# Optimization experiments

Hardware: AMD Instinct MI355X
Metric: run time of the kernel (lower is better)

## Reference

```python
import jax, jax.numpy as jnp
import numpy as np

WS = 3   # window_size
ND = 3   # n_degree


def grid_sample_bilinear(x, grid):
    """torch.nn.functional.grid_sample, mode='bilinear', padding_mode='zeros', align_corners=True.
    x: [B,C,H,W]; grid: [B,Hg,Wg,2] with grid[...,0]=x(norm), grid[...,1]=y(norm). -> [B,C,Hg,Wg]"""
    B, C, H, W = x.shape
    gx = (grid[..., 0] + 1.0) * 0.5 * (W - 1)
    gy = (grid[..., 1] + 1.0) * 0.5 * (H - 1)
    x0 = jnp.floor(gx); y0 = jnp.floor(gy)
    x1 = x0 + 1.0;      y1 = y0 + 1.0
    wx1 = gx - x0; wx0 = 1.0 - wx1
    wy1 = gy - y0; wy0 = 1.0 - wy1
    xf = x.reshape(B, C, H * W)

    def gather(yi, xi):
        valid = ((yi >= 0) & (yi <= H - 1) & (xi >= 0) & (xi <= W - 1)).astype(x.dtype)
        yc = jnp.clip(yi, 0, H - 1).astype(jnp.int32)
        xc = jnp.clip(xi, 0, W - 1).astype(jnp.int32)
        idx = yc * W + xc                                   # [B,Hg,Wg]
        v = jax.vmap(lambda xb, ib: jnp.take(xb, ib, axis=1))(xf, idx.reshape(B, -1))
        v = v.reshape(B, C, idx.shape[1], idx.shape[2])      # [B,C,Hg,Wg]
        return v * valid[:, None]

    out = (gather(y0, x0) * (wy0 * wx0)[:, None]
         + gather(y0, x1) * (wy0 * wx1)[:, None]
         + gather(y1, x0) * (wy1 * wx0)[:, None]
         + gather(y1, x1) * (wy1 * wx1)[:, None])
    return out


def setup_inputs() -> dict:
    key = jax.random.key(0)
    ks = jax.random.split(key, 8)
    B, Q, C, H, W = 16, 500, 256, 64, 64
    Np = ND + 1
    query = jax.random.normal(ks[0], (B, Q, C), dtype=jnp.float32)
    # polynomial coefficients kept small so most sample points land inside [-1,1]
    polys = jax.random.uniform(ks[1], (B, Q, 2 * Np), dtype=jnp.float32, minval=0.0, maxval=0.25)
    memory = jax.random.normal(ks[2], (B, H * W, C), dtype=jnp.float32)
    memory_spatial_shapes = np.array([[H, W]], dtype=np.int64)  # static shapes
    Wk = jax.random.normal(ks[3], (C, Np * C, WS, WS), dtype=jnp.float32) * 0.02
    bk = jax.random.normal(ks[4], (C,), dtype=jnp.float32) * 0.02
    Wp = jax.random.normal(ks[5], (C, C), dtype=jnp.float32) * 0.02
    bp = jax.random.normal(ks[6], (C,), dtype=jnp.float32) * 0.02
    return {"query": query, "polys": polys, "memory": memory,
            "memory_spatial_shapes": memory_spatial_shapes,
            "Wk": Wk, "bk": bk, "Wp": Wp, "bp": bp}


def reference(query, polys, memory, memory_spatial_shapes, Wk, bk, Wp, bp):
    B, LEN_V, C = memory.shape
    H = int(memory_spatial_shapes[0][0]); W = int(memory_spatial_shapes[0][1])
    Q = polys.shape[1]
    Np = ND + 1

    # memory -> feature map [B,C,H,W]
    x = jnp.transpose(memory[:, :H * W, :], (0, 2, 1)).reshape(B, C, H, W)

    # polynomial sample points: alphas[s,k] = linspace(0,1)[s] ** (ND-k)
    a = jnp.linspace(0.0, 1.0, Np).astype(polys.dtype)
    A = jnp.stack([a ** i for i in range(ND, -1, -1)], axis=1)          # [Np, Np]
    pts = jnp.einsum('bqck,sk->bqcs', polys.reshape(B, Q, 2, Np), A)    # [B,Q,2,Np]
    pts = jnp.transpose(pts, (0, 1, 3, 2))[..., ::-1]                   # [B,Q,Np,2] (flip coords)
    points = 2.0 * pts - 1.0
    points = points[:, :, None]                                         # [B,Q,1,Np,2]

    # window offsets (note python floor-div: (-3)//2 = -2, matches torch source)
    delta_h = 2.0 * jnp.linspace((-WS) // 2, WS // 2, WS) / H
    delta_w = 2.0 * jnp.linspace((-WS) // 2, WS // 2, WS) / W
    mesh_x, mesh_y = jnp.meshgrid(delta_w, delta_h, indexing='xy')       # [WS,WS]
    mesh_x = mesh_x.reshape(-1, 1); mesh_y = mesh_y.reshape(-1, 1)       # [WS*WS,1]

    grid_x = points[..., 1] + mesh_x                                     # [B,Q,WS*WS,Np]
    grid_y = points[..., 0] + mesh_y
    grid = jnp.stack((grid_y, grid_x), axis=-1)                          # [B,Q,WS*WS,Np,2]
    grid = grid.reshape(B, Q * Np * WS, WS, 2)

    sampled = grid_sample_bilinear(x, grid)                              # [B,C,Q*Np*WS,WS]
    sampled = sampled.reshape(B, C, Q * Np, WS, WS)
    sampled = jnp.transpose(sampled, (0, 2, 1, 3, 4)).reshape(B * Q, Np * C, WS, WS)

    # convkk over full window -> 1x1 output: plain contraction
    crcts = jax.nn.relu(jnp.einsum('nikl,oikl->no', sampled, Wk) + bk)   # [B*Q, C]
    crcts = (crcts @ Wp.T + bp).reshape(B, Q, C)
    return crcts, points
```

## Files before the change

### kernel.cpp

```cpp
#include <hip/hip_runtime.h>

#define NB 16
#define NQ 500
#define NC 256
#define NHW 64
#define MR 8000
#define KD 9216

typedef float f32x4 __attribute__((ext_vector_type(4)));
typedef __bf16 bf16x8 __attribute__((ext_vector_type(8)));
typedef unsigned short ushortx8 __attribute__((ext_vector_type(8)));
typedef unsigned short ushortx4 __attribute__((ext_vector_type(4)));
typedef int intx4 __attribute__((ext_vector_type(4)));

__device__ __forceinline__ unsigned short f2bf(float f) {
  unsigned int u = __builtin_bit_cast(unsigned int, f);
  u += 0x7fffu + ((u >> 16) & 1u);
  return (unsigned short)(u >> 16);
}
#define BF2F(u) __builtin_bit_cast(float, (unsigned int)((unsigned int)(u) << 16))

__global__ __launch_bounds__(256) void k_cast(const float* __restrict__ mem,
                                              unsigned short* __restrict__ memb) {
  size_t gid = (size_t)blockIdx.x * 256 + threadIdx.x;
  const float* s = mem + gid * 8;
  f32x4 a = *(const f32x4*)s, b = *(const f32x4*)(s + 4);
  bf16x8 pk;
  pk[0] = (__bf16)a.x; pk[1] = (__bf16)a.y; pk[2] = (__bf16)a.z; pk[3] = (__bf16)a.w;
  pk[4] = (__bf16)b.x; pk[5] = (__bf16)b.y; pk[6] = (__bf16)b.z; pk[7] = (__bf16)b.w;
  *(bf16x8*)(memb + gid * 8) = pk;
}

__global__ void k_prew(const float* __restrict__ Wk, const float* __restrict__ Wp,
                       unsigned short* __restrict__ W2s,
                       unsigned short* __restrict__ WPs) {
  int bid = blockIdx.x;
  if (bid < 1152) {
    int tid = bid * 256 + threadIdx.x;
    int o = tid & 255;
    int th = tid >> 8;
    int r = th >> 5;
    int cbase = (th & 31) * 8;
    int np = r / 9;
    int kl = r - np * 9;
    int kk = kl / 3;
    int ll = kl - kk * 3;
    const float* src = Wk + (size_t)o * KD + (size_t)(np * 256 + cbase) * 9 + kk * 3 + ll;
    ushortx8 v;
#pragma unroll
    for (int j = 0; j < 8; ++j) v[j] = f2bf(src[(size_t)j * 9]);
    *(ushortx8*)(W2s + (size_t)th * 2048 + o * 8) = v;
  } else {
    int tid = (bid - 1152) * 256 + threadIdx.x;
    int o = tid & 255;
    int th = tid >> 8;
    const float* src = Wp + (size_t)o * 256 + th * 8;
    ushortx8 v;
#pragma unroll
    for (int j = 0; j < 8; ++j) v[j] = f2bf(src[j]);
    *(ushortx8*)(WPs + (size_t)th * 2048 + o * 8) = v;
  }
}

__global__ void k_wts(const float* __restrict__ polys, float* __restrict__ outp,
                      float* __restrict__ wsp, float* __restrict__ wts) {
  int bid = blockIdx.x;
  if (bid < 1125) {
    if (!wts) return;
    int e = bid * 256 + threadIdx.x;
    int r = e / 8000;
    int n = e - r * 8000;
    int s = r & 3;
    int mm = r >> 2;
    int mdiv = (mm * 11) >> 5;
    int mmod = mm - 3 * mdiv;
    float dhx = (1.5f * (float)mdiv - 2.0f) * 0.03125f;
    float dwy = (1.5f * (float)mmod - 2.0f) * 0.03125f;
    f32x4 ca = *(const f32x4*)(polys + (size_t)n * 8);
    f32x4 cb = *(const f32x4*)(polys + (size_t)n * 8 + 4);
    float a1 = (s == 3) ? 1.0f : (float)s * 0.33333334f;
    float a2 = a1 * a1, a3 = a2 * a1;
    float v0 = ca.x * a3 + ca.y * a2 + ca.z * a1 + ca.w;
    float v1 = cb.x * a3 + cb.y * a2 + cb.z * a1 + cb.w;
    float p0 = 2.0f * v1 - 1.0f;
    float p1 = 2.0f * v0 - 1.0f;
    const float gx = (p0 + dhx + 1.0f) * 0.5f * 63.0f;
    const float gy = (p1 + dwy + 1.0f) * 0.5f * 63.0f;
    const float x0f = floorf(gx), y0f = floorf(gy);
    const float fx = gx - x0f, fy = gy - y0f;
    const int ix0 = (int)x0f, iy0 = (int)y0f;
    const int ix1 = ix0 + 1, iy1 = iy0 + 1;
    const float vx0 = (ix0 >= 0 && ix0 < NHW) ? 1.0f : 0.0f;
    const float vx1 = (ix1 >= 0 && ix1 < NHW) ? 1.0f : 0.0f;
    const float vy0 = (iy0 >= 0 && iy0 < NHW) ? 1.0f : 0.0f;
    const float vy1 = (iy1 >= 0 && iy1 < NHW) ? 1.0f : 0.0f;
    const float w00 = (1.0f - fy) * (1.0f - fx) * vy0 * vx0;
    const float w01 = (1.0f - fy) * fx * vy0 * vx1;
    const float w10 = fy * (1.0f - fx) * vy1 * vx0;
    const float w11 = fy * fx * vy1 * vx1;
    const int cx0 = min(max(ix0, 0), NHW - 1), cx1 = min(max(ix1, 0), NHW - 1);
    const int cy0 = min(max(iy0, 0), NHW - 1), cy1 = min(max(iy1, 0), NHW - 1);
    float* dst = wts + (size_t)e * 8;
    f32x4 wv; wv.x = w00; wv.y = w01; wv.z = w10; wv.w = w11;
    intx4 ov;
    ov.x = (cy0 * NHW + cx0) * NC; ov.y = (cy0 * NHW + cx1) * NC;
    ov.z = (cy1 * NHW + cx0) * NC; ov.w = (cy1 * NHW + cx1) * NC;
    *(f32x4*)dst = wv;
    *(intx4*)(dst + 4) = ov;
  } else {
    int n = (bid - 1125) * 256 + threadIdx.x;
    if (n >= MR) return;
    f32x4 ca = *(const f32x4*)(polys + (size_t)n * 8);
    f32x4 cb = *(const f32x4*)(polys + (size_t)n * 8 + 4);
    const float av[4] = {0.0f, 0.33333334f, 0.66666669f, 1.0f};
#pragma unroll
    for (int s = 0; s < 4; ++s) {
      float a1 = av[s], a2 = a1 * a1, a3 = a2 * a1;
      float v0 = ca.x * a3 + ca.y * a2 + ca.z * a1 + ca.w;
      float v1 = cb.x * a3 + cb.y * a2 + cb.z * a1 + cb.w;
      float pt0 = 2.0f * v1 - 1.0f;
      float pt1 = 2.0f * v0 - 1.0f;
      outp[(size_t)n * 8 + s * 2 + 0] = pt0;
      outp[(size_t)n * 8 + s * 2 + 1] = pt1;
      wsp[(size_t)n * 8 + s * 2 + 0] = pt0;
      wsp[(size_t)n * 8 + s * 2 + 1] = pt1;
    }
  }
}

template <bool USE_WTS>
__global__ __launch_bounds__(512, 4) void k_gemm1(
    const unsigned short* __restrict__ memb, const float* __restrict__ pts,
    const float* __restrict__ wts, const unsigned short* __restrict__ W2s,
    const float* __restrict__ bk, float* __restrict__ PART,
    unsigned short* __restrict__ CR1, int K) {
  __shared__ __align__(16) unsigned short Alds[2 * 2048 * 8];

  const int bid = blockIdx.x;
  const int x = bid & 7;
  const int kk8 = (bid >> 3) % K;
  const int j = bid / (8 * K);
  const int t = x + 8 * j;
  if (t >= 125) return;
  const int tt = 16 * x - ((x > 5) ? (x - 5) : 0) + j;
  const int nsl = 36 / K;
  const int r0 = kk8 * nsl;

  const int tid = threadIdx.x;
  const int n0 = tt * 64;
  const int lane = tid & 63;
  const int wave = tid >> 6;
  const int lr = lane & 15;
  const int ksub = lane >> 4;
  const int o0 = wave * 32;

  const int gchunk = tid & 31;
  const int gm0 = tid >> 5;

  size_t boff[4];
  int nrow[4];
#pragma unroll
  for (int task = 0; task < 4; ++task) {
    nrow[task] = n0 + gm0 + 16 * task;
    boff[task] = (size_t)(nrow[task] / NQ) * (NHW * NHW * NC);
  }

  f32x4 acc[4][2] = {};

  for (int r = r0; r < r0 + nsl; ++r) {
    const int lbase = ((r - r0) & 1) * 2048;
    float dhx = 0.0f, dwy = 0.0f;
    int s = 0;
    if (!USE_WTS) {
      s = r & 3;
      const int mm = r >> 2;
      const int mdiv = (mm * 11) >> 5;
      const int mmod = mm - 3 * mdiv;
      dhx = (1.5f * (float)mdiv - 2.0f) * 0.03125f;
      dwy = (1.5f * (float)mmod - 2.0f) * 0.03125f;
    }
#pragma unroll 2
    for (int task = 0; task < 4; ++task) {
      const int m = gm0 + task * 16;
      const int n = nrow[task];
      float w00, w01, w10, w11;
      int o00, o01, o10, o11;
      if (USE_WTS) {
        const float* we = wts + ((size_t)r * 8000 + n) * 8;
        f32x4 wv = *(const f32x4*)we;
        intx4 ov = *(const intx4*)(we + 4);
        w00 = wv.x; w01 = wv.y; w10 = wv.z; w11 = wv.w;
        o00 = ov.x; o01 = ov.y; o10 = ov.z; o11 = ov.w;
      } else {
        const float p0 = pts[(size_t)n * 8 + s * 2 + 0];
        const float p1 = pts[(size_t)n * 8 + s * 2 + 1];
        const float gx = (p0 + dhx + 1.0f) * 0.5f * 63.0f;
        const float gy = (p1 + dwy + 1.0f) * 0.5f * 63.0f;
        const float x0f = floorf(gx), y0f = floorf(gy);
        const float fx = gx - x0f, fy = gy - y0f;
        const int ix0 = (int)x0f, iy0 = (int)y0f;
        const int ix1 = ix0 + 1, iy1 = iy0 + 1;
        const float vx0 = (ix0 >= 0 && ix0 < NHW) ? 1.0f : 0.0f;
        const float vx1 = (ix1 >= 0 && ix1 < NHW) ? 1.0f : 0.0f;
        const float vy0 = (iy0 >= 0 && iy0 < NHW) ? 1.0f : 0.0f;
        const float vy1 = (iy1 >= 0 && iy1 < NHW) ? 1.0f : 0.0f;
        w00 = (1.0f - fy) * (1.0f - fx) * vy0 * vx0;
        w01 = (1.0f - fy) * fx * vy0 * vx1;
        w10 = fy * (1.0f - fx) * vy1 * vx0;
        w11 = fy * fx * vy1 * vx1;
        const int cx0 = min(max(ix0, 0), NHW - 1), cx1 = min(max(ix1, 0), NHW - 1);
        const int cy0 = min(max(iy0, 0), NHW - 1), cy1 = min(max(iy1, 0), NHW - 1);
        o00 = (cy0 * NHW + cx0) * NC; o01 = (cy0 * NHW + cx1) * NC;
        o10 = (cy1 * NHW + cx0) * NC; o11 = (cy1 * NHW + cx1) * NC;
      }
      const unsigned short* mb = memb + boff[task] + gchunk * 8;
      ushortx8 u00 = *(const ushortx8*)(mb + o00);
      ushortx8 u01 = *(const ushortx8*)(mb + o01);
      ushortx8 u10 = *(const ushortx8*)(mb + o10);
      ushortx8 u11 = *(const ushortx8*)(mb + o11);
      f32x4 ra, rb;
#pragma unroll
      for (int jj = 0; jj < 4; ++jj) {
        ra[jj] = BF2F(u00[jj]) * w00 + BF2F(u01[jj]) * w01 +
                 BF2F(u10[jj]) * w10 + BF2F(u11[jj]) * w11;
        rb[jj] = BF2F(u00[jj + 4]) * w00 + BF2F(u01[jj + 4]) * w01 +
                 BF2F(u10[jj + 4]) * w10 + BF2F(u11[jj + 4]) * w11;
      }
      bf16x8 pk;
      pk[0] = (__bf16)ra.x; pk[1] = (__bf16)ra.y;
      pk[2] = (__bf16)ra.z; pk[3] = (__bf16)ra.w;
      pk[4] = (__bf16)rb.x; pk[5] = (__bf16)rb.y;
      pk[6] = (__bf16)rb.z; pk[7] = (__bf16)rb.w;
      const int slot = lbase + gchunk * 64 + (m ^ (gchunk & 15));
      *(bf16x8*)(Alds + slot * 8) = pk;
    }
    __syncthreads();
    const size_t rbase = (size_t)r * 32;
#pragma unroll
    for (int kstep = 0; kstep < 8; ++kstep) {
      const int chunk = kstep * 4 + ksub;
      const unsigned short* bp = W2s + (rbase + chunk) * 2048 + (o0 + lr) * 8;
      ushortx8 ub0 = *(const ushortx8*)bp;
      ushortx8 ub1 = *(const ushortx8*)(bp + 128);
      bf16x8 fb0 = __builtin_bit_cast(bf16x8, ub0);
      bf16x8 fb1 = __builtin_bit_cast(bf16x8, ub1);
#pragma unroll
      for (int mf = 0; mf < 4; ++mf) {
        const int sa = lbase + chunk * 64 + ((mf * 16 + lr) ^ (chunk & 15));
        ushortx8 ua = *(const ushortx8*)(Alds + sa * 8);
        bf16x8 fa = __builtin_bit_cast(bf16x8, ua);
        acc[mf][0] = __builtin_amdgcn_mfma_f32_16x16x32_bf16(fa, fb0, acc[mf][0], 0, 0, 0);
        acc[mf][1] = __builtin_amdgcn_mfma_f32_16x16x32_bf16(fa, fb1, acc[mf][1], 0, 0, 0);
      }
    }
  }
  if (PART) {
    float* dst = PART + (size_t)kk8 * (MR * NC);
#pragma unroll
    for (int mf = 0; mf < 4; ++mf)
#pragma unroll
      for (int nf = 0; nf < 2; ++nf) {
        const int o = o0 + nf * 16 + lr;
#pragma unroll
        for (int reg = 0; reg < 4; ++reg) {
          const int mrow = mf * 16 + ksub * 4 + reg;
          dst[(size_t)(n0 + mrow) * 256 + o] = acc[mf][nf][reg];
        }
      }
  } else {
#pragma unroll
    for (int mf = 0; mf < 4; ++mf)
#pragma unroll
      for (int nf = 0; nf < 2; ++nf) {
        const int o = o0 + nf * 16 + lr;
        const float bko = bk[o];
#pragma unroll
        for (int reg = 0; reg < 4; ++reg) {
          const int mrow = mf * 16 + ksub * 4 + reg;
          float v = acc[mf][nf][reg] + bko;
          v = v > 0.0f ? v : 0.0f;
          CR1[(size_t)(n0 + mrow) * 256 + o] = f2bf(v);
        }
      }
  }
}

__global__ __launch_bounds__(256) void k_red(
    const float* __restrict__ PART, const float* __restrict__ bk,
    unsigned short* __restrict__ CR1, int K) {
  int gid = blockIdx.x * 256 + threadIdx.x;
  size_t idx4 = (size_t)gid * 4;
  if (idx4 >= (size_t)MR * NC) return;
  f32x4 sum = *(const f32x4*)(PART + idx4);
  for (int k = 1; k < K; ++k)
    sum += *(const f32x4*)(PART + (size_t)k * (MR * NC) + idx4);
  f32x4 bv = *(const f32x4*)(bk + (idx4 & 255));
  sum += bv;
  ushortx4 pk;
#pragma unroll
  for (int e = 0; e < 4; ++e) {
    float v = sum[e] > 0.0f ? sum[e] : 0.0f;
    pk[e] = f2bf(v);
  }
  *(ushortx4*)(CR1 + idx4) = pk;
}

__global__ __launch_bounds__(256) void k_gemm2(
    const unsigned short* __restrict__ CR1, const unsigned short* __restrict__ WPs,
    const float* __restrict__ bp, float* __restrict__ outc) {
  const int tid = threadIdx.x;
  const int n0 = blockIdx.x * 16;
  const int lane = tid & 63;
  const int wave = tid >> 6;
  const int lr = lane & 15;
  const int ksub = lane >> 4;
  const int o0 = wave * 64;
  f32x4 acc[4] = {};
#pragma unroll
  for (int kstep = 0; kstep < 8; ++kstep) {
    const int t0 = kstep * 32 + ksub * 8;
    ushortx8 ua0 = *(const ushortx8*)(CR1 + (size_t)(n0 + lr) * 256 + t0);
    bf16x8 fa0 = __builtin_bit_cast(bf16x8, ua0);
    const int chunk = kstep * 4 + ksub;
#pragma unroll
    for (int nf = 0; nf < 4; ++nf) {
      ushortx8 ub = *(const ushortx8*)(WPs + (size_t)chunk * 2048 + (o0 + nf * 16 + lr) * 8);
      bf16x8 fb = __builtin_bit_cast(bf16x8, ub);
      acc[nf] = __builtin_amdgcn_mfma_f32_16x16x32_bf16(fa0, fb, acc[nf], 0, 0, 0);
    }
  }
#pragma unroll
  for (int nf = 0; nf < 4; ++nf) {
    const int o = o0 + nf * 16 + lr;
    const float bpo = bp[o];
#pragma unroll
    for (int reg = 0; reg < 4; ++reg) {
      const int mrow = ksub * 4 + reg;
      outc[(size_t)(n0 + mrow) * 256 + o] = acc[nf][reg] + bpo;
    }
  }
}

extern "C" void kernel_launch(void* const* d_in, const int* in_sizes, int n_in,
                              void* d_out, int out_size, void* d_ws, size_t ws_size,
                              hipStream_t stream) {
  (void)in_sizes; (void)n_in; (void)out_size;
  const float* polys = (const float*)d_in[1];
  const float* mem   = (const float*)d_in[2];
  const float* Wk    = (const float*)d_in[4];
  const float* bk    = (const float*)d_in[5];
  const float* Wp    = (const float*)d_in[6];
  const float* bp    = (const float*)d_in[7];
  float* out = (float*)d_out;
  float* out_pts = out + (size_t)MR * NC;

  unsigned short* W2s = (unsigned short*)d_ws;
  unsigned short* WPs = (unsigned short*)((char*)d_ws + 4718592);
  float*          PTS = (float*)((char*)d_ws + 4849664);
  unsigned short* CR1 = (unsigned short*)((char*)d_ws + 5105664);
  const size_t BASE_END = 9201664;
  const size_t WTS_SZ  = 9216000ull;
  const size_t MEMB_SZ = 33554432ull;
  const size_t PART_SZ = 8192000ull;
  const int K = 4;

  bool use_wts = (ws_size >= BASE_END + WTS_SZ + MEMB_SZ + 4 * PART_SZ);
  size_t memb_off = use_wts ? (BASE_END + WTS_SZ) : BASE_END;
  float*          WTS  = use_wts ? (float*)((char*)d_ws + BASE_END) : nullptr;
  unsigned short* MEMB = (unsigned short*)((char*)d_ws + memb_off);
  float*          PART = (float*)((char*)d_ws + memb_off + MEMB_SZ);

  hipLaunchKernelGGL(k_wts, dim3(1157), dim3(256), 0, stream, polys, out_pts, PTS, WTS);
  hipLaunchKernelGGL(k_cast, dim3(8192), dim3(256), 0, stream, mem, MEMB);
  hipLaunchKernelGGL(k_prew, dim3(1184), dim3(256), 0, stream, Wk, Wp, W2s, WPs);
  if (use_wts)
    hipLaunchKernelGGL(k_gemm1<true>, dim3(128 * K), dim3(512), 0, stream,
                       MEMB, PTS, WTS, W2s, bk, PART, CR1, K);
  else
    hipLaunchKernelGGL(k_gemm1<false>, dim3(128 * K), dim3(512), 0, stream,
                       MEMB, PTS, WTS, W2s, bk, PART, CR1, K);
  hipLaunchKernelGGL(k_red, dim3(2000), dim3(256), 0, stream, PART, bk, CR1, K);
  hipLaunchKernelGGL(k_gemm2, dim3(500), dim3(256), 0, stream, CR1, WPs, bp, out);
}
```

Measured before the change: 110.8 us.

## Merge prep kernels, fuse split-K reduction into second GEMM, vectorize bf16 unpack

The three preprocessing kernels (memory cast, weight repack, sample weights) become one launch that dispatches on block index. The split-K partial reduction, bias, ReLU and bf16 conversion move into the A-operand load of the second GEMM, which removes the separate reduction kernel and the CR1 round trip. The bilinear gather now unpacks bf16 pairs with 32-bit shifts and masks and uses vector FMAs. In exchange, k_gemm2 reads four fp32 partial buffers directly, so its per-block load volume grows, and the non-PART epilogue path in gemm1 is dropped.

```diff
diff --git a/kernel.cpp b/kernel.cpp
--- a/kernel.cpp
+++ b/kernel.cpp
@@ -10,7 +10,7 @@
 typedef float f32x4 __attribute__((ext_vector_type(4)));
 typedef __bf16 bf16x8 __attribute__((ext_vector_type(8)));
 typedef unsigned short ushortx8 __attribute__((ext_vector_type(8)));
-typedef unsigned short ushortx4 __attribute__((ext_vector_type(4)));
+typedef unsigned int uintx4 __attribute__((ext_vector_type(4)));
 typedef int intx4 __attribute__((ext_vector_type(4)));
 
 __device__ __forceinline__ unsigned short f2bf(float f) {
@@ -18,25 +18,24 @@
   u += 0x7fffu + ((u >> 16) & 1u);
   return (unsigned short)(u >> 16);
 }
-#define BF2F(u) __builtin_bit_cast(float, (unsigned int)((unsigned int)(u) << 16))
-
-__global__ __launch_bounds__(256) void k_cast(const float* __restrict__ mem,
-                                              unsigned short* __restrict__ memb) {
-  size_t gid = (size_t)blockIdx.x * 256 + threadIdx.x;
-  const float* s = mem + gid * 8;
-  f32x4 a = *(const f32x4*)s, b = *(const f32x4*)(s + 4);
-  bf16x8 pk;
-  pk[0] = (__bf16)a.x; pk[1] = (__bf16)a.y; pk[2] = (__bf16)a.z; pk[3] = (__bf16)a.w;
-  pk[4] = (__bf16)b.x; pk[5] = (__bf16)b.y; pk[6] = (__bf16)b.z; pk[7] = (__bf16)b.w;
-  *(bf16x8*)(memb + gid * 8) = pk;
-}
-
-__global__ void k_prew(const float* __restrict__ Wk, const float* __restrict__ Wp,
-                       unsigned short* __restrict__ W2s,
-                       unsigned short* __restrict__ WPs) {
-  int bid = blockIdx.x;
-  if (bid < 1152) {
-    int tid = bid * 256 + threadIdx.x;
+#define U2F(u) __builtin_bit_cast(float, (unsigned int)(u))
+
+__global__ void k_prep(const float* __restrict__ mem, unsigned short* __restrict__ memb,
+                       const float* __restrict__ Wk, const float* __restrict__ Wp,
+                       unsigned short* __restrict__ W2s, unsigned short* __restrict__ WPs,
+                       const float* __restrict__ polys, float* __restrict__ outp,
+                       float* __restrict__ wsp, float* __restrict__ wts) {
+  const int bid = blockIdx.x;
+  if (bid < 8192) {
+    size_t gid = (size_t)bid * 256 + threadIdx.x;
+    const float* s = mem + gid * 8;
+    f32x4 a = *(const f32x4*)s, b = *(const f32x4*)(s + 4);
+    bf16x8 pk;
+    pk[0] = (__bf16)a.x; pk[1] = (__bf16)a.y; pk[2] = (__bf16)a.z; pk[3] = (__bf16)a.w;
+    pk[4] = (__bf16)b.x; pk[5] = (__bf16)b.y; pk[6] = (__bf16)b.z; pk[7] = (__bf16)b.w;
+    *(bf16x8*)(memb + gid * 8) = pk;
+  } else if (bid < 9344) {
+    int tid = (bid - 8192) * 256 + threadIdx.x;
     int o = tid & 255;
     int th = tid >> 8;
     int r = th >> 5;
@@ -50,8 +49,8 @@
 #pragma unroll
     for (int j = 0; j < 8; ++j) v[j] = f2bf(src[(size_t)j * 9]);
     *(ushortx8*)(W2s + (size_t)th * 2048 + o * 8) = v;
-  } else {
-    int tid = (bid - 1152) * 256 + threadIdx.x;
+  } else if (bid < 9376) {
+    int tid = (bid - 9344) * 256 + threadIdx.x;
     int o = tid & 255;
     int th = tid >> 8;
     const float* src = Wp + (size_t)o * 256 + th * 8;
@@ -59,15 +58,9 @@
 #pragma unroll
     for (int j = 0; j < 8; ++j) v[j] = f2bf(src[j]);
     *(ushortx8*)(WPs + (size_t)th * 2048 + o * 8) = v;
-  }
-}
-
-__global__ void k_wts(const float* __restrict__ polys, float* __restrict__ outp,
-                      float* __restrict__ wsp, float* __restrict__ wts) {
-  int bid = blockIdx.x;
-  if (bid < 1125) {
+  } else if (bid < 10501) {
     if (!wts) return;
-    int e = bid * 256 + threadIdx.x;
+    int e = (bid - 9376) * 256 + threadIdx.x;
     int r = e / 8000;
     int n = e - r * 8000;
     int s = r & 3;
@@ -108,7 +101,7 @@
     *(f32x4*)dst = wv;
     *(intx4*)(dst + 4) = ov;
   } else {
-    int n = (bid - 1125) * 256 + threadIdx.x;
+    int n = (bid - 10501) * 256 + threadIdx.x;
     if (n >= MR) return;
     f32x4 ca = *(const f32x4*)(polys + (size_t)n * 8);
     f32x4 cb = *(const f32x4*)(polys + (size_t)n * 8 + 4);
@@ -132,8 +125,7 @@
 __global__ __launch_bounds__(512, 4) void k_gemm1(
     const unsigned short* __restrict__ memb, const float* __restrict__ pts,
     const float* __restrict__ wts, const unsigned short* __restrict__ W2s,
-    const float* __restrict__ bk, float* __restrict__ PART,
-    unsigned short* __restrict__ CR1, int K) {
+    const float* __restrict__ bk, float* __restrict__ PART, int K) {
   __shared__ __align__(16) unsigned short Alds[2 * 2048 * 8];
 
   const int bid = blockIdx.x;
@@ -214,18 +206,29 @@
         o10 = (cy1 * NHW + cx0) * NC; o11 = (cy1 * NHW + cx1) * NC;
       }
       const unsigned short* mb = memb + boff[task] + gchunk * 8;
-      ushortx8 u00 = *(const ushortx8*)(mb + o00);
-      ushortx8 u01 = *(const ushortx8*)(mb + o01);
-      ushortx8 u10 = *(const ushortx8*)(mb + o10);
-      ushortx8 u11 = *(const ushortx8*)(mb + o11);
-      f32x4 ra, rb;
-#pragma unroll
-      for (int jj = 0; jj < 4; ++jj) {
-        ra[jj] = BF2F(u00[jj]) * w00 + BF2F(u01[jj]) * w01 +
-                 BF2F(u10[jj]) * w10 + BF2F(u11[jj]) * w11;
-        rb[jj] = BF2F(u00[jj + 4]) * w00 + BF2F(u01[jj + 4]) * w01 +
-                 BF2F(u10[jj + 4]) * w10 + BF2F(u11[jj + 4]) * w11;
-      }
+      uintx4 u00 = *(const uintx4*)(mb + o00);
+      uintx4 u01 = *(const uintx4*)(mb + o01);
+      uintx4 u10 = *(const uintx4*)(mb + o10);
+      uintx4 u11 = *(const uintx4*)(mb + o11);
+      f32x4 a00, b00, a01, b01, a10, b10, a11, b11;
+      a00.x = U2F(u00.x << 16); a00.y = U2F(u00.x & 0xFFFF0000u);
+      a00.z = U2F(u00.y << 16); a00.w = U2F(u00.y & 0xFFFF0000u);
+      b00.x = U2F(u00.z << 16); b00.y = U2F(u00.z & 0xFFFF0000u);
+      b00.z = U2F(u00.w << 16); b00.w = U2F(u00.w & 0xFFFF0000u);
+      a01.x = U2F(u01.x << 16); a01.y = U2F(u01.x & 0xFFFF0000u);
+      a01.z = U2F(u01.y << 16); a01.w = U2F(u01.y & 0xFFFF0000u);
+      b01.x = U2F(u01.z << 16); b01.y = U2F(u01.z & 0xFFFF0000u);
+      b01.z = U2F(u01.w << 16); b01.w = U2F(u01.w & 0xFFFF0000u);
+      a10.x = U2F(u10.x << 16); a10.y = U2F(u10.x & 0xFFFF0000u);
+      a10.z = U2F(u10.y << 16); a10.w = U2F(u10.y & 0xFFFF0000u);
+      b10.x = U2F(u10.z << 16); b10.y = U2F(u10.z & 0xFFFF0000u);
+      b10.z = U2F(u10.w << 16); b10.w = U2F(u10.w & 0xFFFF0000u);
+      a11.x = U2F(u11.x << 16); a11.y = U2F(u11.x & 0xFFFF0000u);
+      a11.z = U2F(u11.y << 16); a11.w = U2F(u11.y & 0xFFFF0000u);
+      b11.x = U2F(u11.z << 16); b11.y = U2F(u11.z & 0xFFFF0000u);
+      b11.z = U2F(u11.w << 16); b11.w = U2F(u11.w & 0xFFFF0000u);
+      f32x4 ra = a00 * w00 + a01 * w01 + a10 * w10 + a11 * w11;
+      f32x4 rb = b00 * w00 + b01 * w01 + b10 * w10 + b11 * w11;
       bf16x8 pk;
       pk[0] = (__bf16)ra.x; pk[1] = (__bf16)ra.y;
       pk[2] = (__bf16)ra.z; pk[3] = (__bf16)ra.w;
@@ -254,60 +257,24 @@
       }
     }
   }
-  if (PART) {
-    float* dst = PART + (size_t)kk8 * (MR * NC);
-#pragma unroll
-    for (int mf = 0; mf < 4; ++mf)
-#pragma unroll
-      for (int nf = 0; nf < 2; ++nf) {
-        const int o = o0 + nf * 16 + lr;
-#pragma unroll
-        for (int reg = 0; reg < 4; ++reg) {
-          const int mrow = mf * 16 + ksub * 4 + reg;
-          dst[(size_t)(n0 + mrow) * 256 + o] = acc[mf][nf][reg];
-        }
+  float* dst = PART + (size_t)kk8 * (MR * NC);
+#pragma unroll
+  for (int mf = 0; mf < 4; ++mf)
+#pragma unroll
+    for (int nf = 0; nf < 2; ++nf) {
+      const int o = o0 + nf * 16 + lr;
+#pragma unroll
+      for (int reg = 0; reg < 4; ++reg) {
+        const int mrow = mf * 16 + ksub * 4 + reg;
+        dst[(size_t)(n0 + mrow) * 256 + o] = acc[mf][nf][reg];
       }
-  } else {
-#pragma unroll
-    for (int mf = 0; mf < 4; ++mf)
-#pragma unroll
-      for (int nf = 0; nf < 2; ++nf) {
-        const int o = o0 + nf * 16 + lr;
-        const float bko = bk[o];
-#pragma unroll
-        for (int reg = 0; reg < 4; ++reg) {
-          const int mrow = mf * 16 + ksub * 4 + reg;
-          float v = acc[mf][nf][reg] + bko;
-          v = v > 0.0f ? v : 0.0f;
-          CR1[(size_t)(n0 + mrow) * 256 + o] = f2bf(v);
-        }
-      }
-  }
-}
-
-__global__ __launch_bounds__(256) void k_red(
+    }
+}
+
+__global__ __launch_bounds__(256) void k_gemm2(
     const float* __restrict__ PART, const float* __restrict__ bk,
-    unsigned short* __restrict__ CR1, int K) {
-  int gid = blockIdx.x * 256 + threadIdx.x;
-  size_t idx4 = (size_t)gid * 4;
-  if (idx4 >= (size_t)MR * NC) return;
-  f32x4 sum = *(const f32x4*)(PART + idx4);
-  for (int k = 1; k < K; ++k)
-    sum += *(const f32x4*)(PART + (size_t)k * (MR * NC) + idx4);
-  f32x4 bv = *(const f32x4*)(bk + (idx4 & 255));
-  sum += bv;
-  ushortx4 pk;
-#pragma unroll
-  for (int e = 0; e < 4; ++e) {
-    float v = sum[e] > 0.0f ? sum[e] : 0.0f;
-    pk[e] = f2bf(v);
-  }
-  *(ushortx4*)(CR1 + idx4) = pk;
-}
-
-__global__ __launch_bounds__(256) void k_gemm2(
-    const unsigned short* __restrict__ CR1, const unsigned short* __restrict__ WPs,
-    const float* __restrict__ bp, float* __restrict__ outc) {
+    const unsigned short* __restrict__ WPs, const float* __restrict__ bp,
+    float* __restrict__ outc) {
   const int tid = threadIdx.x;
   const int n0 = blockIdx.x * 16;
   const int lane = tid & 63;
@@ -319,14 +286,31 @@
 #pragma unroll
   for (int kstep = 0; kstep < 8; ++kstep) {
     const int t0 = kstep * 32 + ksub * 8;
-    ushortx8 ua0 = *(const ushortx8*)(CR1 + (size_t)(n0 + lr) * 256 + t0);
-    bf16x8 fa0 = __builtin_bit_cast(bf16x8, ua0);
+    const float* base = PART + (size_t)(n0 + lr) * 256 + t0;
+    f32x4 s0 = *(const f32x4*)base;
+    f32x4 s1 = *(const f32x4*)(base + 4);
+#pragma unroll
+    for (int k = 1; k < 4; ++k) {
+      const float* pk_ = base + (size_t)k * (MR * NC);
+      s0 += *(const f32x4*)pk_;
+      s1 += *(const f32x4*)(pk_ + 4);
+    }
+    s0 += *(const f32x4*)(bk + t0);
+    s1 += *(const f32x4*)(bk + t0 + 4);
+    bf16x8 fa;
+#pragma unroll
+    for (int e = 0; e < 4; ++e) {
+      float v0 = s0[e] > 0.0f ? s0[e] : 0.0f;
+      float v1 = s1[e] > 0.0f ? s1[e] : 0.0f;
+      fa[e] = (__bf16)v0;
+      fa[e + 4] = (__bf16)v1;
+    }
     const int chunk = kstep * 4 + ksub;
 #pragma unroll
     for (int nf = 0; nf < 4; ++nf) {
       ushortx8 ub = *(const ushortx8*)(WPs + (size_t)chunk * 2048 + (o0 + nf * 16 + lr) * 8);
       bf16x8 fb = __builtin_bit_cast(bf16x8, ub);
-      acc[nf] = __builtin_amdgcn_mfma_f32_16x16x32_bf16(fa0, fb, acc[nf], 0, 0, 0);
+      acc[nf] = __builtin_amdgcn_mfma_f32_16x16x32_bf16(fa, fb, acc[nf], 0, 0, 0);
     }
   }
 #pragma unroll
@@ -357,7 +341,6 @@
   unsigned short* W2s = (unsigned short*)d_ws;
   unsigned short* WPs = (unsigned short*)((char*)d_ws + 4718592);
   float*          PTS = (float*)((char*)d_ws + 4849664);
-  unsigned short* CR1 = (unsigned short*)((char*)d_ws + 5105664);
   const size_t BASE_END = 9201664;
   const size_t WTS_SZ  = 9216000ull;
   const size_t MEMB_SZ = 33554432ull;
@@ -370,15 +353,13 @@
   unsigned short* MEMB = (unsigned short*)((char*)d_ws + memb_off);
   float*          PART = (float*)((char*)d_ws + memb_off + MEMB_SZ);
 
-  hipLaunchKernelGGL(k_wts, dim3(1157), dim3(256), 0, stream, polys, out_pts, PTS, WTS);
-  hipLaunchKernelGGL(k_cast, dim3(8192), dim3(256), 0, stream, mem, MEMB);
-  hipLaunchKernelGGL(k_prew, dim3(1184), dim3(256), 0, stream, Wk, Wp, W2s, WPs);
+  hipLaunchKernelGGL(k_prep, dim3(10533), dim3(256), 0, stream,
+                     mem, MEMB, Wk, Wp, W2s, WPs, polys, out_pts, PTS, WTS);
   if (use_wts)
     hipLaunchKernelGGL(k_gemm1<true>, dim3(128 * K), dim3(512), 0, stream,
-                       MEMB, PTS, WTS, W2s, bk, PART, CR1, K);
+                       MEMB, PTS, WTS, W2s, bk, PART, K);
   else
     hipLaunchKernelGGL(k_gemm1<false>, dim3(128 * K), dim3(512), 0, stream,
-                       MEMB, PTS, WTS, W2s, bk, PART, CR1, K);
-  hipLaunchKernelGGL(k_red, dim3(2000), dim3(256), 0, stream, PART, bk, CR1, K);
-  hipLaunchKernelGGL(k_gemm2, dim3(500), dim3(256), 0, stream, CR1, WPs, bp, out);
-}
+                       MEMB, PTS, WTS, W2s, bk, PART, K);
+  hipLaunchKernelGGL(k_gemm2, dim3(500), dim3(256), 0, stream, PART, bk, WPs, bp, out);
+}
```

Result: no change. 109.8 us (-0.9%).
